# Optimization experiments

Measured on AMD Instinct MI355X. Metric: run time of the kernel, lower is better.

## Reference

```python
import jax, jax.numpy as jnp
import numpy as np

N_NODES = 100000


def setup_inputs() -> dict:
    key = jax.random.key(0)
    k1, k2, k3, k4, k5 = jax.random.split(key, 5)
    h = jax.random.normal(k1, (N_NODES, 128), dtype=jnp.float32)
    norm = jax.random.uniform(k2, (N_NODES, 1), dtype=jnp.float32)  # D^{-1/2}-style per-node norm
    W = jax.random.normal(k3, (128, 64), dtype=jnp.float32) * 0.05
    b = jnp.zeros((64,), dtype=jnp.float32)
    src = jax.random.randint(k4, (1600000,), 0, N_NODES, dtype=jnp.int32)
    dst = jax.random.randint(k5, (1600000,), 0, N_NODES, dtype=jnp.int32)
    return {"h": h, "norm": norm, "W": W, "b": b, "src": src, "dst": dst}


def reference(h, norm, W, b, src, dst):
    # Dense feature transform: g.ndata['h'] = h @ W   (dropout is identity at inference)
    hw = jnp.matmul(h, W)  # [N, out]
    # Message: src feature scaled by src norm
    msg = hw[src] * norm[src]  # [E, out]
    # Reduce: sum messages into dst, scale by dst norm
    agg = jax.ops.segment_sum(msg, dst, num_segments=N_NODES) * norm  # [N, out]
    out = agg + b
    return jax.nn.relu(out)
```

## Files before the change

kernel.cpp:

```cpp
#include <hip/hip_runtime.h>


typedef unsigned int u32;
typedef unsigned short u16;
typedef __attribute__((ext_vector_type(8))) short s16x8;
typedef __attribute__((ext_vector_type(4))) float f32x4;

#define NB_LOG 6
#define NPB 64
#define CAP 2048
#define MAXB 2048
#define EPB 8192
#define RT 256

__device__ __forceinline__ float bf2f(u16 v) {
  return __uint_as_float(((u32)v) << 16);
}
__device__ __forceinline__ u16 f2bf(float f) {
  u32 u = __float_as_uint(f);
  return (u16)((u + 0x7fffu + ((u >> 16) & 1u)) >> 16);
}
__device__ __forceinline__ void acc_bf16x4(float4& a, uint2 v) {
  a.x += __uint_as_float(v.x << 16);
  a.y += __uint_as_float(v.x & 0xFFFF0000u);
  a.z += __uint_as_float(v.y << 16);
  a.w += __uint_as_float(v.y & 0xFFFF0000u);
}

__global__ __launch_bounds__(256) void wconv(
    const float* __restrict__ W, u16* __restrict__ Wtg, u32* __restrict__ gcur) {
  int o = blockIdx.x * 256 + threadIdx.x;
  int j = o & 7, col = (o >> 3) & 15, kq = (o >> 7) & 3, ks = (o >> 9) & 3,
      ct = (o >> 11) & 3;
  int k = ks * 32 + kq * 8 + j;
  int n = ct * 16 + col;
  Wtg[o] = f2bf(W[k * 64 + n]);
  if (o < MAXB) gcur[o] = 0;
}

__global__ __launch_bounds__(256) void gemm_mfma(
    const float* __restrict__ h, const float* __restrict__ norm,
    const u16* __restrict__ Wtg, u16* __restrict__ scaledh, int N) {
  int lane = threadIdx.x & 63, wid = threadIdx.x >> 6;
  int col = lane & 15, kq = lane >> 4;

  s16x8 bfrag[4][4];
#pragma unroll
  for (int ct = 0; ct < 4; ++ct)
#pragma unroll
    for (int ks = 0; ks < 4; ++ks) {
      int f = ct * 16 + ks * 4 + kq;
      bfrag[ct][ks] =
          *reinterpret_cast<const s16x8*>(Wtg + ((size_t)(f * 16 + col) * 8));
    }

  int row0 = blockIdx.x * 64 + wid * 16;
  int myrow = row0 + col;
  int ldrow = myrow < N ? myrow : (N - 1);
  const float* __restrict__ hrow = h + (size_t)ldrow * 128 + kq * 8;

  f32x4 acc[4];
#pragma unroll
  for (int ct = 0; ct < 4; ++ct) acc[ct] = (f32x4){0.f, 0.f, 0.f, 0.f};

#pragma unroll
  for (int ks = 0; ks < 4; ++ks) {
    float4 x0 = *reinterpret_cast<const float4*>(hrow + ks * 32);
    float4 x1 = *reinterpret_cast<const float4*>(hrow + ks * 32 + 4);
    s16x8 a;
    a[0] = (short)f2bf(x0.x); a[1] = (short)f2bf(x0.y);
    a[2] = (short)f2bf(x0.z); a[3] = (short)f2bf(x0.w);
    a[4] = (short)f2bf(x1.x); a[5] = (short)f2bf(x1.y);
    a[6] = (short)f2bf(x1.z); a[7] = (short)f2bf(x1.w);
#pragma unroll
    for (int ct = 0; ct < 4; ++ct)
      acc[ct] =
          __builtin_amdgcn_mfma_f32_16x16x32_bf16(a, bfrag[ct][ks], acc[ct], 0, 0, 0);
  }

#pragma unroll
  for (int reg = 0; reg < 4; ++reg) {
    int node = row0 + kq * 4 + reg;
    if (node < N) {
      float nm = norm[node];
#pragma unroll
      for (int ct = 0; ct < 4; ++ct)
        scaledh[(size_t)node * 64 + ct * 16 + col] = f2bf(acc[ct][reg] * nm);
    }
  }
}

__global__ __launch_bounds__(1024) void bin_edges(
    const int* __restrict__ src, const int* __restrict__ dst,
    u32* __restrict__ gcur, u32* __restrict__ bins, int E) {
  __shared__ u32 lhist[MAXB];
  __shared__ u32 lbase[MAXB];
  int t = threadIdx.x;
  for (int i = t; i < MAXB; i += 1024) lhist[i] = 0;
  __syncthreads();
  int e0 = blockIdx.x * EPB;
  int s[8], d[8];
  u32 r[8];
#pragma unroll
  for (int k = 0; k < 8; ++k) {
    int e = e0 + k * 1024 + t;
    bool ok = e < E;
    s[k] = ok ? src[e] : 0;
    d[k] = ok ? dst[e] : -1;
  }
#pragma unroll
  for (int k = 0; k < 8; ++k) {
    if (d[k] >= 0) r[k] = atomicAdd(&lhist[d[k] >> NB_LOG], 1u);
  }
  __syncthreads();
  for (int i = t; i < MAXB; i += 1024) {
    u32 c = lhist[i];
    lbase[i] = c ? atomicAdd(&gcur[i], c) : 0u;
  }
  __syncthreads();
#pragma unroll
  for (int k = 0; k < 8; ++k) {
    if (d[k] >= 0) {
      int bk = d[k] >> NB_LOG;
      u32 p = lbase[bk] + r[k];
      if (p < CAP)
        bins[(size_t)bk * CAP + p] = ((u32)s[k] << NB_LOG) | (u32)(d[k] & (NPB - 1));
    }
  }
}

__global__ __launch_bounds__(RT) void bucket_reduce(
    const u16* __restrict__ scaledh, const u32* __restrict__ bins,
    const u32* __restrict__ gcur, const float* __restrict__ norm,
    const float4* __restrict__ bias4, float* __restrict__ out, int N) {
  __shared__ u32 hist[NPB];
  __shared__ u32 startp[NPB + 1];
  __shared__ u32 sorted[CAP];
  int bkt = blockIdx.x;
  int t = threadIdx.x, lane = t & 63, wid = t >> 6;
  int cnt = (int)gcur[bkt];
  if (cnt > CAP) cnt = CAP;
  if (t < NPB) hist[t] = 0;
  __syncthreads();

  const u32* __restrict__ my = bins + (size_t)bkt * CAP;
  u32 w[CAP / RT];
  u32 rk[CAP / RT];
#pragma unroll
  for (int k = 0; k < CAP / RT; ++k) {
    int e = k * RT + t;
    w[k] = (e < cnt) ? my[e] : 0xFFFFFFFFu;
  }
#pragma unroll
  for (int k = 0; k < CAP / RT; ++k) {
    if (w[k] != 0xFFFFFFFFu)
      rk[k] = atomicAdd(&hist[w[k] & (NPB - 1)], 1u);
  }
  __syncthreads();
  if (t < NPB) {
    u32 v = hist[t];
    u32 inc = v;
#pragma unroll
    for (int m = 1; m < NPB; m <<= 1) {
      u32 x = __shfl_up(inc, m);
      if (t >= m) inc += x;
    }
    startp[t] = inc - v;
    if (t == NPB - 1) startp[NPB] = inc;
  }
  __syncthreads();
#pragma unroll
  for (int k = 0; k < CAP / RT; ++k) {
    if (w[k] != 0xFFFFFFFFu)
      sorted[startp[w[k] & (NPB - 1)] + rk[k]] = w[k] >> NB_LOG;
  }
  __syncthreads();

  int grp = lane >> 4, c4 = lane & 15;
  float4 bl = bias4[c4];
  int base = bkt << NB_LOG;
  int cm1 = cnt - 1;
#pragma unroll
  for (int round = 0; round < 2; ++round) {
    int rA = (wid << 4) + (round << 3) + grp;
    int rB = rA + 4;
    int jA = (int)startp[rA], eA = (int)startp[rA + 1];
    int jB = (int)startp[rB], eB = (int)startp[rB + 1];
    float4 aA = make_float4(0.f, 0.f, 0.f, 0.f);
    float4 aB = make_float4(0.f, 0.f, 0.f, 0.f);
    while (jA < eA || jB < eB) {
      int iA0 = (int)sorted[min(jA, cm1)];
      int iA1 = (int)sorted[min(jA + 1, cm1)];
      int iB0 = (int)sorted[min(jB, cm1)];
      int iB1 = (int)sorted[min(jB + 1, cm1)];
      uint2 vA0 = *reinterpret_cast<const uint2*>(scaledh + ((size_t)iA0 << 6) + (c4 << 2));
      uint2 vA1 = *reinterpret_cast<const uint2*>(scaledh + ((size_t)iA1 << 6) + (c4 << 2));
      uint2 vB0 = *reinterpret_cast<const uint2*>(scaledh + ((size_t)iB0 << 6) + (c4 << 2));
      uint2 vB1 = *reinterpret_cast<const uint2*>(scaledh + ((size_t)iB1 << 6) + (c4 << 2));
      uint2 z = make_uint2(0u, 0u);
      vA0 = (jA < eA) ? vA0 : z;
      vA1 = (jA + 1 < eA) ? vA1 : z;
      vB0 = (jB < eB) ? vB0 : z;
      vB1 = (jB + 1 < eB) ? vB1 : z;
      acc_bf16x4(aA, vA0);
      acc_bf16x4(aA, vA1);
      acc_bf16x4(aB, vB0);
      acc_bf16x4(aB, vB1);
      jA += 2;
      jB += 2;
    }
    int nodeA = base + rA, nodeB = base + rB;
    if (nodeA < N) {
      float nm = norm[nodeA];
      float4 o;
      o.x = fmaxf(fmaf(aA.x, nm, bl.x), 0.f);
      o.y = fmaxf(fmaf(aA.y, nm, bl.y), 0.f);
      o.z = fmaxf(fmaf(aA.z, nm, bl.z), 0.f);
      o.w = fmaxf(fmaf(aA.w, nm, bl.w), 0.f);
      *reinterpret_cast<float4*>(out + (size_t)nodeA * 64 + (c4 << 2)) = o;
    }
    if (nodeB < N) {
      float nm = norm[nodeB];
      float4 o;
      o.x = fmaxf(fmaf(aB.x, nm, bl.x), 0.f);
      o.y = fmaxf(fmaf(aB.y, nm, bl.y), 0.f);
      o.z = fmaxf(fmaf(aB.z, nm, bl.z), 0.f);
      o.w = fmaxf(fmaf(aB.w, nm, bl.w), 0.f);
      *reinterpret_cast<float4*>(out + (size_t)nodeB * 64 + (c4 << 2)) = o;
    }
  }
}

__global__ __launch_bounds__(256) void zero_out(float4* __restrict__ o4, size_t n4) {
  size_t tid = blockIdx.x * 256 + threadIdx.x;
  size_t stride = (size_t)gridDim.x * 256;
  for (size_t i = tid; i < n4; i += stride) o4[i] = make_float4(0.f, 0.f, 0.f, 0.f);
}

__global__ __launch_bounds__(256) void scatter_edges(
    const u16* __restrict__ scaledh, const int* __restrict__ src,
    const int* __restrict__ dst, float* __restrict__ agg, int E) {
  int lane = threadIdx.x & 63;
  int gwid = (blockIdx.x * 256 + threadIdx.x) >> 6;
  int nw = (gridDim.x * 256) >> 6;
  for (int e = gwid; e < E; e += nw) {
    int s = __builtin_amdgcn_readfirstlane(src[e]);
    int d = __builtin_amdgcn_readfirstlane(dst[e]);
    float v = bf2f(scaledh[(size_t)s * 64 + lane]);
    unsafeAtomicAdd(&agg[(size_t)d * 64 + lane], v);
  }
}

__global__ __launch_bounds__(256) void finalize(
    float4* __restrict__ out4, const float* __restrict__ norm,
    const float4* __restrict__ b4, int N) {
  size_t total4 = (size_t)N * 16;
  size_t tid = blockIdx.x * 256 + threadIdx.x;
  size_t stride = (size_t)gridDim.x * 256;
  for (size_t t = tid; t < total4; t += stride) {
    int i = (int)(t >> 4), q = (int)(t & 15);
    float4 v = out4[t];
    float nm = norm[i];
    float4 bb = b4[q];
    v.x = fmaxf(fmaf(v.x, nm, bb.x), 0.f);
    v.y = fmaxf(fmaf(v.y, nm, bb.y), 0.f);
    v.z = fmaxf(fmaf(v.z, nm, bb.z), 0.f);
    v.w = fmaxf(fmaf(v.w, nm, bb.w), 0.f);
    out4[t] = v;
  }
}

extern "C" void kernel_launch(void* const* d_in, const int* in_sizes, int n_in,
                              void* d_out, int out_size, void* d_ws, size_t ws_size,
                              hipStream_t stream) {
  const float* h    = (const float*)d_in[0];
  const float* norm = (const float*)d_in[1];
  const float* W    = (const float*)d_in[2];
  const float* b    = (const float*)d_in[3];
  const int*   src  = (const int*)d_in[4];
  const int*   dst  = (const int*)d_in[5];

  int N = in_sizes[1];
  int E = in_sizes[4];
  int nbuckets = (N + NPB - 1) >> NB_LOG;
  int nrb = (N + 63) >> 6;
  int nbinb = (E + EPB - 1) / EPB;

  char* ws = (char*)d_ws;
  size_t off = 0;
  u16* scaledh = (u16*)(ws + off); off += (((size_t)N * 64 * 2) + 255) & ~(size_t)255;
  u32* gcur    = (u32*)(ws + off); off += (MAXB * 4 + 255) & ~(size_t)255;
  u16* Wtg     = (u16*)(ws + off); off += (8192 * 2 + 255) & ~(size_t)255;
  u32* bins    = (u32*)(ws + off); off += (size_t)MAXB * CAP * 4;
  size_t needed = off;
  size_t needed_fb = (size_t)((char*)bins - ws);

  if (ws_size >= needed && nbuckets <= MAXB) {
    wconv<<<32, 256, 0, stream>>>(W, Wtg, gcur);
    gemm_mfma<<<nrb, 256, 0, stream>>>(h, norm, Wtg, scaledh, N);
    bin_edges<<<nbinb, 1024, 0, stream>>>(src, dst, gcur, bins, E);
    bucket_reduce<<<nbuckets, RT, 0, stream>>>(scaledh, bins, gcur, norm,
                                               (const float4*)b, (float*)d_out, N);
  } else if (ws_size >= needed_fb) {
    float* agg = (float*)d_out;
    wconv<<<32, 256, 0, stream>>>(W, Wtg, gcur);
    gemm_mfma<<<nrb, 256, 0, stream>>>(h, norm, Wtg, scaledh, N);
    zero_out<<<1024, 256, 0, stream>>>((float4*)agg, (size_t)N * 16);
    scatter_edges<<<2048, 256, 0, stream>>>(scaledh, src, dst, agg, E);
    finalize<<<1024, 256, 0, stream>>>((float4*)agg, norm, (const float4*)b, N);
  }
}
```

Baseline: 80.06 us.

## Widen bucket_reduce gathers to 16-byte loads with 4-edge unrolled loops

Reworks the gather-reduce phase so each lane loads 8 bf16 features (uint4) instead of 4, using 8 lanes per node and handling 16 nodes per wave in one pass rather than two rounds. The inner loop is unrolled by 4 edges with split accumulators, and separate tail loops plus a padded shared index array replace the per-iteration clamping and masking. The goal is more bytes per memory instruction and more loads in flight per lane to hide gather latency. In exchange it uses more registers per thread and more code, which can lower occupancy, and imbalanced degrees between the paired nodes fall into serial tail loops.

Result: slower. 90.47 us (+13.0%).

```diff
diff --git a/kernel.cpp b/kernel.cpp
--- a/kernel.cpp
+++ b/kernel.cpp
@@ -20,11 +20,15 @@
   u32 u = __float_as_uint(f);
   return (u16)((u + 0x7fffu + ((u >> 16) & 1u)) >> 16);
 }
-__device__ __forceinline__ void acc_bf16x4(float4& a, uint2 v) {
-  a.x += __uint_as_float(v.x << 16);
-  a.y += __uint_as_float(v.x & 0xFFFF0000u);
-  a.z += __uint_as_float(v.y << 16);
-  a.w += __uint_as_float(v.y & 0xFFFF0000u);
+__device__ __forceinline__ void acc_bf16x8(float4& lo, float4& hi, uint4 v) {
+  lo.x += __uint_as_float(v.x << 16);
+  lo.y += __uint_as_float(v.x & 0xFFFF0000u);
+  lo.z += __uint_as_float(v.y << 16);
+  lo.w += __uint_as_float(v.y & 0xFFFF0000u);
+  hi.x += __uint_as_float(v.z << 16);
+  hi.y += __uint_as_float(v.z & 0xFFFF0000u);
+  hi.z += __uint_as_float(v.w << 16);
+  hi.w += __uint_as_float(v.w & 0xFFFF0000u);
 }
 
 __global__ __launch_bounds__(256) void wconv(
@@ -132,10 +136,10 @@
 __global__ __launch_bounds__(RT) void bucket_reduce(
     const u16* __restrict__ scaledh, const u32* __restrict__ bins,
     const u32* __restrict__ gcur, const float* __restrict__ norm,
-    const float4* __restrict__ bias4, float* __restrict__ out, int N) {
+    const float* __restrict__ bias, float* __restrict__ out, int N) {
   __shared__ u32 hist[NPB];
   __shared__ u32 startp[NPB + 1];
-  __shared__ u32 sorted[CAP];
+  __shared__ u32 sorted[CAP + 4];
   int bkt = blockIdx.x;
   int t = threadIdx.x, lane = t & 63, wid = t >> 6;
   int cnt = (int)gcur[bkt];
@@ -174,60 +178,126 @@
     if (w[k] != 0xFFFFFFFFu)
       sorted[startp[w[k] & (NPB - 1)] + rk[k]] = w[k] >> NB_LOG;
   }
-  __syncthreads();
-
-  int grp = lane >> 4, c4 = lane & 15;
-  float4 bl = bias4[c4];
+  if (t < 4) sorted[cnt + t] = 0;
+  __syncthreads();
+
+  int grp = lane >> 3, c8 = lane & 7;
+  float4 bl0 = *reinterpret_cast<const float4*>(bias + c8 * 8);
+  float4 bl1 = *reinterpret_cast<const float4*>(bias + c8 * 8 + 4);
   int base = bkt << NB_LOG;
-  int cm1 = cnt - 1;
-#pragma unroll
-  for (int round = 0; round < 2; ++round) {
-    int rA = (wid << 4) + (round << 3) + grp;
-    int rB = rA + 4;
-    int jA = (int)startp[rA], eA = (int)startp[rA + 1];
-    int jB = (int)startp[rB], eB = (int)startp[rB + 1];
-    float4 aA = make_float4(0.f, 0.f, 0.f, 0.f);
-    float4 aB = make_float4(0.f, 0.f, 0.f, 0.f);
-    while (jA < eA || jB < eB) {
-      int iA0 = (int)sorted[min(jA, cm1)];
-      int iA1 = (int)sorted[min(jA + 1, cm1)];
-      int iB0 = (int)sorted[min(jB, cm1)];
-      int iB1 = (int)sorted[min(jB + 1, cm1)];
-      uint2 vA0 = *reinterpret_cast<const uint2*>(scaledh + ((size_t)iA0 << 6) + (c4 << 2));
-      uint2 vA1 = *reinterpret_cast<const uint2*>(scaledh + ((size_t)iA1 << 6) + (c4 << 2));
-      uint2 vB0 = *reinterpret_cast<const uint2*>(scaledh + ((size_t)iB0 << 6) + (c4 << 2));
-      uint2 vB1 = *reinterpret_cast<const uint2*>(scaledh + ((size_t)iB1 << 6) + (c4 << 2));
-      uint2 z = make_uint2(0u, 0u);
-      vA0 = (jA < eA) ? vA0 : z;
-      vA1 = (jA + 1 < eA) ? vA1 : z;
-      vB0 = (jB < eB) ? vB0 : z;
-      vB1 = (jB + 1 < eB) ? vB1 : z;
-      acc_bf16x4(aA, vA0);
-      acc_bf16x4(aA, vA1);
-      acc_bf16x4(aB, vB0);
-      acc_bf16x4(aB, vB1);
-      jA += 2;
-      jB += 2;
-    }
-    int nodeA = base + rA, nodeB = base + rB;
-    if (nodeA < N) {
-      float nm = norm[nodeA];
-      float4 o;
-      o.x = fmaxf(fmaf(aA.x, nm, bl.x), 0.f);
-      o.y = fmaxf(fmaf(aA.y, nm, bl.y), 0.f);
-      o.z = fmaxf(fmaf(aA.z, nm, bl.z), 0.f);
-      o.w = fmaxf(fmaf(aA.w, nm, bl.w), 0.f);
-      *reinterpret_cast<float4*>(out + (size_t)nodeA * 64 + (c4 << 2)) = o;
-    }
-    if (nodeB < N) {
-      float nm = norm[nodeB];
-      float4 o;
-      o.x = fmaxf(fmaf(aB.x, nm, bl.x), 0.f);
-      o.y = fmaxf(fmaf(aB.y, nm, bl.y), 0.f);
-      o.z = fmaxf(fmaf(aB.z, nm, bl.z), 0.f);
-      o.w = fmaxf(fmaf(aB.w, nm, bl.w), 0.f);
-      *reinterpret_cast<float4*>(out + (size_t)nodeB * 64 + (c4 << 2)) = o;
-    }
+  const u16* __restrict__ sh = scaledh + (c8 << 3);
+
+  int rA = (wid << 4) + grp;
+  int rB = rA + 8;
+  int jA = (int)startp[rA], eA = (int)startp[rA + 1];
+  int jB = (int)startp[rB], eB = (int)startp[rB + 1];
+  float4 aA0l = {0,0,0,0}, aA0h = {0,0,0,0}, aA1l = {0,0,0,0}, aA1h = {0,0,0,0};
+  float4 aB0l = {0,0,0,0}, aB0h = {0,0,0,0}, aB1l = {0,0,0,0}, aB1h = {0,0,0,0};
+
+  while (jA + 4 <= eA && jB + 4 <= eB) {
+    int iA0 = (int)sorted[jA], iA1 = (int)sorted[jA + 1],
+        iA2 = (int)sorted[jA + 2], iA3 = (int)sorted[jA + 3];
+    int iB0 = (int)sorted[jB], iB1 = (int)sorted[jB + 1],
+        iB2 = (int)sorted[jB + 2], iB3 = (int)sorted[jB + 3];
+    uint4 vA0 = *reinterpret_cast<const uint4*>(sh + ((size_t)iA0 << 6));
+    uint4 vA1 = *reinterpret_cast<const uint4*>(sh + ((size_t)iA1 << 6));
+    uint4 vA2 = *reinterpret_cast<const uint4*>(sh + ((size_t)iA2 << 6));
+    uint4 vA3 = *reinterpret_cast<const uint4*>(sh + ((size_t)iA3 << 6));
+    uint4 vB0 = *reinterpret_cast<const uint4*>(sh + ((size_t)iB0 << 6));
+    uint4 vB1 = *reinterpret_cast<const uint4*>(sh + ((size_t)iB1 << 6));
+    uint4 vB2 = *reinterpret_cast<const uint4*>(sh + ((size_t)iB2 << 6));
+    uint4 vB3 = *reinterpret_cast<const uint4*>(sh + ((size_t)iB3 << 6));
+    acc_bf16x8(aA0l, aA0h, vA0);
+    acc_bf16x8(aA1l, aA1h, vA1);
+    acc_bf16x8(aA0l, aA0h, vA2);
+    acc_bf16x8(aA1l, aA1h, vA3);
+    acc_bf16x8(aB0l, aB0h, vB0);
+    acc_bf16x8(aB1l, aB1h, vB1);
+    acc_bf16x8(aB0l, aB0h, vB2);
+    acc_bf16x8(aB1l, aB1h, vB3);
+    jA += 4;
+    jB += 4;
+  }
+  while (jA + 4 <= eA) {
+    int i0 = (int)sorted[jA], i1 = (int)sorted[jA + 1],
+        i2 = (int)sorted[jA + 2], i3 = (int)sorted[jA + 3];
+    uint4 v0 = *reinterpret_cast<const uint4*>(sh + ((size_t)i0 << 6));
+    uint4 v1 = *reinterpret_cast<const uint4*>(sh + ((size_t)i1 << 6));
+    uint4 v2 = *reinterpret_cast<const uint4*>(sh + ((size_t)i2 << 6));
+    uint4 v3 = *reinterpret_cast<const uint4*>(sh + ((size_t)i3 << 6));
+    acc_bf16x8(aA0l, aA0h, v0);
+    acc_bf16x8(aA1l, aA1h, v1);
+    acc_bf16x8(aA0l, aA0h, v2);
+    acc_bf16x8(aA1l, aA1h, v3);
+    jA += 4;
+  }
+  while (jB + 4 <= eB) {
+    int i0 = (int)sorted[jB], i1 = (int)sorted[jB + 1],
+        i2 = (int)sorted[jB + 2], i3 = (int)sorted[jB + 3];
+    uint4 v0 = *reinterpret_cast<const uint4*>(sh + ((size_t)i0 << 6));
+    uint4 v1 = *reinterpret_cast<const uint4*>(sh + ((size_t)i1 << 6));
+    uint4 v2 = *reinterpret_cast<const uint4*>(sh + ((size_t)i2 << 6));
+    uint4 v3 = *reinterpret_cast<const uint4*>(sh + ((size_t)i3 << 6));
+    acc_bf16x8(aB0l, aB0h, v0);
+    acc_bf16x8(aB1l, aB1h, v1);
+    acc_bf16x8(aB0l, aB0h, v2);
+    acc_bf16x8(aB1l, aB1h, v3);
+    jB += 4;
+  }
+  if (jA < eA || jB < eB) {
+    int iA0 = (int)sorted[jA], iA1 = (int)sorted[jA + 1], iA2 = (int)sorted[jA + 2];
+    int iB0 = (int)sorted[jB], iB1 = (int)sorted[jB + 1], iB2 = (int)sorted[jB + 2];
+    uint4 vA0 = *reinterpret_cast<const uint4*>(sh + ((size_t)iA0 << 6));
+    uint4 vA1 = *reinterpret_cast<const uint4*>(sh + ((size_t)iA1 << 6));
+    uint4 vA2 = *reinterpret_cast<const uint4*>(sh + ((size_t)iA2 << 6));
+    uint4 vB0 = *reinterpret_cast<const uint4*>(sh + ((size_t)iB0 << 6));
+    uint4 vB1 = *reinterpret_cast<const uint4*>(sh + ((size_t)iB1 << 6));
+    uint4 vB2 = *reinterpret_cast<const uint4*>(sh + ((size_t)iB2 << 6));
+    uint4 z = make_uint4(0u, 0u, 0u, 0u);
+    vA0 = (jA + 0 < eA) ? vA0 : z;
+    vA1 = (jA + 1 < eA) ? vA1 : z;
+    vA2 = (jA + 2 < eA) ? vA2 : z;
+    vB0 = (jB + 0 < eB) ? vB0 : z;
+    vB1 = (jB + 1 < eB) ? vB1 : z;
+    vB2 = (jB + 2 < eB) ? vB2 : z;
+    acc_bf16x8(aA0l, aA0h, vA0);
+    acc_bf16x8(aA1l, aA1h, vA1);
+    acc_bf16x8(aA0l, aA0h, vA2);
+    acc_bf16x8(aB0l, aB0h, vB0);
+    acc_bf16x8(aB1l, aB1h, vB1);
+    acc_bf16x8(aB0l, aB0h, vB2);
+  }
+
+  int nodeA = base + rA, nodeB = base + rB;
+  if (nodeA < N) {
+    float nm = norm[nodeA];
+    float4 o0, o1;
+    o0.x = fmaxf(fmaf(aA0l.x + aA1l.x, nm, bl0.x), 0.f);
+    o0.y = fmaxf(fmaf(aA0l.y + aA1l.y, nm, bl0.y), 0.f);
+    o0.z = fmaxf(fmaf(aA0l.z + aA1l.z, nm, bl0.z), 0.f);
+    o0.w = fmaxf(fmaf(aA0l.w + aA1l.w, nm, bl0.w), 0.f);
+    o1.x = fmaxf(fmaf(aA0h.x + aA1h.x, nm, bl1.x), 0.f);
+    o1.y = fmaxf(fmaf(aA0h.y + aA1h.y, nm, bl1.y), 0.f);
+    o1.z = fmaxf(fmaf(aA0h.z + aA1h.z, nm, bl1.z), 0.f);
+    o1.w = fmaxf(fmaf(aA0h.w + aA1h.w, nm, bl1.w), 0.f);
+    float* op = out + (size_t)nodeA * 64 + c8 * 8;
+    *reinterpret_cast<float4*>(op) = o0;
+    *reinterpret_cast<float4*>(op + 4) = o1;
+  }
+  if (nodeB < N) {
+    float nm = norm[nodeB];
+    float4 o0, o1;
+    o0.x = fmaxf(fmaf(aB0l.x + aB1l.x, nm, bl0.x), 0.f);
+    o0.y = fmaxf(fmaf(aB0l.y + aB1l.y, nm, bl0.y), 0.f);
+    o0.z = fmaxf(fmaf(aB0l.z + aB1l.z, nm, bl0.z), 0.f);
+    o0.w = fmaxf(fmaf(aB0l.w + aB1l.w, nm, bl0.w), 0.f);
+    o1.x = fmaxf(fmaf(aB0h.x + aB1h.x, nm, bl1.x), 0.f);
+    o1.y = fmaxf(fmaf(aB0h.y + aB1h.y, nm, bl1.y), 0.f);
+    o1.z = fmaxf(fmaf(aB0h.z + aB1h.z, nm, bl1.z), 0.f);
+    o1.w = fmaxf(fmaf(aB0h.w + aB1h.w, nm, bl1.w), 0.f);
+    float* op = out + (size_t)nodeB * 64 + c8 * 8;
+    *reinterpret_cast<float4*>(op) = o0;
+    *reinterpret_cast<float4*>(op + 4) = o1;
   }
 }
 
@@ -300,7 +370,7 @@
     gemm_mfma<<<nrb, 256, 0, stream>>>(h, norm, Wtg, scaledh, N);
     bin_edges<<<nbinb, 1024, 0, stream>>>(src, dst, gcur, bins, E);
     bucket_reduce<<<nbuckets, RT, 0, stream>>>(scaledh, bins, gcur, norm,
-                                               (const float4*)b, (float*)d_out, N);
+                                               b, (float*)d_out, N);
   } else if (ws_size >= needed_fb) {
     float* agg = (float*)d_out;
     wconv<<<32, 256, 0, stream>>>(W, Wtg, gcur);
```
